# Performance work log

Hardware: AMD Instinct MI355X
Metric: run time of the kernel (lower is better)

Reference implementation:

```python
import jax, jax.numpy as jnp
import numpy as np
from jax import lax

NUM_HEADS = 4
SIDE = 5  # side_dwconv


def setup_inputs() -> dict:
    key = jax.random.key(0)
    ks = jax.random.split(key, 7)
    B, C, H, W = 2, 128, 56, 56
    return {
        "x": jax.random.normal(ks[0], (B, C, H, W), dtype=jnp.float32),
        "qkv_w": jax.random.normal(ks[1], (3 * C, C), dtype=jnp.float32) * 0.02,
        "qkv_b": jax.random.normal(ks[2], (3 * C,), dtype=jnp.float32) * 0.02,
        "lepe_w": jax.random.normal(ks[3], (C, 1, SIDE, SIDE), dtype=jnp.float32) * 0.02,
        "lepe_b": jax.random.normal(ks[4], (C,), dtype=jnp.float32) * 0.02,
        "proj_w": jax.random.normal(ks[5], (C, C), dtype=jnp.float32) * 0.02,
        "proj_b": jax.random.normal(ks[6], (C,), dtype=jnp.float32) * 0.02,
    }


def reference(x, qkv_w, qkv_b, lepe_w, lepe_b, proj_w, proj_b):
    B, C, H, W = x.shape
    nh = NUM_HEADS
    hd = C // nh
    scale = hd ** (-0.5)
    N = H * W

    # 1x1 conv qkv == channel matmul
    qkv = jnp.einsum('oc,bchw->bohw', qkv_w, x) + qkv_b[None, :, None, None]
    q, k, v = jnp.split(qkv, 3, axis=1)  # each [B, C, H, W]

    qr = q.reshape(B, nh, hd, N)
    kr = k.reshape(B, nh, hd, N)
    vr = v.reshape(B, nh, hd, N)

    # attn = q^T k over head_dim -> [B, nh, N, N]
    attn = jnp.einsum('bhdn,bhdm->bhnm', qr, kr) * scale
    attn = jax.nn.softmax(attn, axis=-1)

    # out = attn @ v^T, then permute back to [B, C, H, W]
    out = jnp.einsum('bhnm,bhdm->bhdn', attn, vr).reshape(B, C, H, W)

    # depthwise LePE conv on v, fused with residual add
    pad = SIDE // 2
    lepe = lax.conv_general_dilated(
        v, lepe_w, window_strides=(1, 1), padding=[(pad, pad), (pad, pad)],
        dimension_numbers=('NCHW', 'OIHW', 'NCHW'), feature_group_count=C,
    ) + lepe_b[None, :, None, None]
    out = out + lepe

    # 1x1 conv proj
    out = jnp.einsum('oc,bchw->bohw', proj_w, out) + proj_b[None, :, None, None]
    return out
```

## Files before the change

### kernel.cpp

```cpp
#include <hip/hip_runtime.h>

typedef __bf16 bf16x8 __attribute__((ext_vector_type(8)));
typedef __bf16 bf16x4 __attribute__((ext_vector_type(4)));
typedef float  f32x4  __attribute__((ext_vector_type(4)));

#define NPIX  3136
#define WIMG  56
#define CCH   128
#define NH    4
#define HD    32
#define NSPLIT 8
#define QSCALE 0.2550565470841439f

#if __has_builtin(__builtin_amdgcn_exp2f)
#define FEXP2(x) __builtin_amdgcn_exp2f(x)
#else
#define FEXP2(x) __expf((x) * 0.6931471805599453f)
#endif


__device__ __forceinline__ int perm_inv(int k) {
    return (((k >> 5) & 1) * 2 + ((k >> 2) & 1)) * 16 + (((k >> 3) & 3) * 4) + (k & 3);
}

__global__ __launch_bounds__(256) void k_qkv(
    const float* __restrict__ x, const float* __restrict__ qkv_w,
    const float* __restrict__ qkv_b,
    __bf16* __restrict__ qT, __bf16* __restrict__ kT,
    __bf16* __restrict__ vT, __bf16* __restrict__ vP)
{
    __shared__ __bf16 xl[64][136];
    const int tid = threadIdx.x;
    const int w = tid >> 6, lane = tid & 63;
    const int col = lane & 15, g = lane >> 4;
    const int px0 = blockIdx.x * 64;
    const int slab = blockIdx.y;
    const int b = blockIdx.z;
    const int obase = slab * 128 + w * 32;

    {
        const int px = tid & 63, cq = tid >> 6;
        const float* xp = x + (size_t)b * CCH * NPIX + px0 + px;
        #pragma unroll
        for (int i = 0; i < 8; ++i) {
            const int c0 = cq * 4 + i * 16;
            const float v0 = xp[(size_t)(c0 + 0) * NPIX];
            const float v1 = xp[(size_t)(c0 + 1) * NPIX];
            const float v2 = xp[(size_t)(c0 + 2) * NPIX];
            const float v3 = xp[(size_t)(c0 + 3) * NPIX];
            bf16x4 bv = {(__bf16)v0, (__bf16)v1, (__bf16)v2, (__bf16)v3};
            *(bf16x4*)&xl[px][c0] = bv;
        }
    }
    __syncthreads();

    f32x4 acc[2][4];
    #pragma unroll
    for (int ot = 0; ot < 2; ++ot)
        #pragma unroll
        for (int a = 0; a < 4; ++a) acc[ot][a] = (f32x4){0.f, 0.f, 0.f, 0.f};

    #pragma unroll
    for (int ks = 0; ks < 4; ++ks) {
        const int c0 = ks * 32 + g * 8;
        #pragma unroll
        for (int ot = 0; ot < 2; ++ot) {
            const float* wrow = qkv_w + (size_t)(obase + ot * 16 + col) * CCH + c0;
            const float4 wA = *(const float4*)(wrow);
            const float4 wB = *(const float4*)(wrow + 4);
            bf16x8 af = {(__bf16)wA.x, (__bf16)wA.y, (__bf16)wA.z, (__bf16)wA.w,
                         (__bf16)wB.x, (__bf16)wB.y, (__bf16)wB.z, (__bf16)wB.w};
            #pragma unroll
            for (int a = 0; a < 4; ++a) {
                const bf16x8 bf_ = *(const bf16x8*)&xl[16 * a + col][c0];
                acc[ot][a] = __builtin_amdgcn_mfma_f32_16x16x32_bf16(af, bf_, acc[ot][a], 0, 0, 0);
            }
        }
    }

    #pragma unroll
    for (int ot = 0; ot < 2; ++ot) {
        const int orow = obase + ot * 16 + g * 4;
        const f32x4 bias4 = *(const f32x4*)(qkv_b + orow);
        if (slab == 0) {
            const int o = orow, h = o >> 5, d0 = o & 31;
            __bf16* dst = qT + ((size_t)(b * NH + h) * NPIX) * HD + d0;
            #pragma unroll
            for (int a = 0; a < 4; ++a) {
                const int px = px0 + 16 * a + col;
                bf16x4 v;
                #pragma unroll
                for (int r = 0; r < 4; ++r) v[r] = (__bf16)((acc[ot][a][r] + bias4[r]) * QSCALE);
                *(bf16x4*)(dst + (size_t)px * HD) = v;
            }
        } else if (slab == 1) {
            const int o = orow - 128, h = o >> 5, d0 = o & 31;
            __bf16* dst = kT + ((size_t)(b * NH + h) * NPIX) * HD + d0;
            #pragma unroll
            for (int a = 0; a < 4; ++a) {
                const int s = perm_inv(16 * a + col);
                bf16x4 v;
                #pragma unroll
                for (int r = 0; r < 4; ++r) v[r] = (__bf16)(acc[ot][a][r] + bias4[r]);
                *(bf16x4*)(dst + (size_t)(px0 + s) * HD) = v;
            }
        } else {
            const int c = orow - 256;
            #pragma unroll
            for (int a = 0; a < 4; ++a) {
                const int px = px0 + 16 * a + col;
                const int s = perm_inv(16 * a + col);
                bf16x4 v;
                #pragma unroll
                for (int r = 0; r < 4; ++r) v[r] = (__bf16)(acc[ot][a][r] + bias4[r]);
                *(bf16x4*)(vT + ((size_t)(b * NPIX + px)) * CCH + c) = v;
                #pragma unroll
                for (int r = 0; r < 4; ++r)
                    vP[((size_t)(b * CCH + c + r)) * NPIX + px0 + s] = v[r];
            }
        }
    }
}

__global__ __launch_bounds__(256) void k_attn(
    const __bf16* __restrict__ qT, const __bf16* __restrict__ kT,
    const __bf16* __restrict__ vP,
    __bf16* __restrict__ pO, float* __restrict__ pl)
{
    const int tid = threadIdx.x;
    const int w = tid >> 6, lane = tid & 63;
    const int col = lane & 15, g = lane >> 4;
    const int qt = blockIdx.x;
    const int bh = blockIdx.y;
    const int sp = blockIdx.z * 4 + w;
    const int b = bh >> 2, h = bh & 3;
    const int qbase = qt * 64;
    const size_t headoff = (size_t)bh * NPIX * HD;
    const int c0h = h * HD;

    const __bf16* qbp = qT + headoff + (size_t)(qbase + col) * HD + g * 8;
    const bf16x8 aq0 = *(const bf16x8*)(qbp);
    const bf16x8 aq1 = *(const bf16x8*)(qbp + 16 * HD);
    const bf16x8 aq2 = *(const bf16x8*)(qbp + 32 * HD);
    const bf16x8 aq3 = *(const bf16x8*)(qbp + 48 * HD);

    const __bf16 one = (__bf16)1.0f;
    const bf16x8 ones = {one, one, one, one, one, one, one, one};

    f32x4 O00 = {0,0,0,0}, O01 = {0,0,0,0}, O10 = {0,0,0,0}, O11 = {0,0,0,0};
    f32x4 O20 = {0,0,0,0}, O21 = {0,0,0,0}, O30 = {0,0,0,0}, O31 = {0,0,0,0};
    f32x4 La0 = {0,0,0,0}, La1 = {0,0,0,0}, La2 = {0,0,0,0}, La3 = {0,0,0,0};

    const __bf16* kTh   = kT + headoff;
    const __bf16* vrow0 = vP + (size_t)(b * CCH + c0h + col)      * NPIX;
    const __bf16* vrow1 = vP + (size_t)(b * CCH + c0h + 16 + col) * NPIX;

    const int cs = (49 * sp) >> 3, ce = (49 * (sp + 1)) >> 3;

#define LOADK4(K0R, K1R, K2R, K3R, CHUNK) do { const int _k0 = (CHUNK) * 64;           \
        K0R = *(const bf16x8*)(kTh + (size_t)(_k0      + col) * HD + g * 8);           \
        K1R = *(const bf16x8*)(kTh + (size_t)(_k0 + 16 + col) * HD + g * 8);           \
        K2R = *(const bf16x8*)(kTh + (size_t)(_k0 + 32 + col) * HD + g * 8);           \
        K3R = *(const bf16x8*)(kTh + (size_t)(_k0 + 48 + col) * HD + g * 8); } while (0)

#define SQH(AQ, O0R, O1R, LAR)  do {                                                   \
        f32x4 s0 = __builtin_amdgcn_mfma_f32_16x16x32_bf16(ck0, AQ, zz, 0, 0, 0);      \
        f32x4 s1 = __builtin_amdgcn_mfma_f32_16x16x32_bf16(ck1, AQ, zz, 0, 0, 0);      \
        f32x4 s2 = __builtin_amdgcn_mfma_f32_16x16x32_bf16(ck2, AQ, zz, 0, 0, 0);      \
        f32x4 s3 = __builtin_amdgcn_mfma_f32_16x16x32_bf16(ck3, AQ, zz, 0, 0, 0);      \
        bf16x8 P0 = {(__bf16)FEXP2(s0[0]), (__bf16)FEXP2(s0[1]),                       \
                     (__bf16)FEXP2(s0[2]), (__bf16)FEXP2(s0[3]),                       \
                     (__bf16)FEXP2(s1[0]), (__bf16)FEXP2(s1[1]),                       \
                     (__bf16)FEXP2(s1[2]), (__bf16)FEXP2(s1[3])};                      \
        bf16x8 P1 = {(__bf16)FEXP2(s2[0]), (__bf16)FEXP2(s2[1]),                       \
                     (__bf16)FEXP2(s2[2]), (__bf16)FEXP2(s2[3]),                       \
                     (__bf16)FEXP2(s3[0]), (__bf16)FEXP2(s3[1]),                       \
                     (__bf16)FEXP2(s3[2]), (__bf16)FEXP2(s3[3])};                      \
        O0R = __builtin_amdgcn_mfma_f32_16x16x32_bf16(vv00, P0, O0R, 0, 0, 0);         \
        O0R = __builtin_amdgcn_mfma_f32_16x16x32_bf16(vv01, P1, O0R, 0, 0, 0);         \
        O1R = __builtin_amdgcn_mfma_f32_16x16x32_bf16(vv10, P0, O1R, 0, 0, 0);         \
        O1R = __builtin_amdgcn_mfma_f32_16x16x32_bf16(vv11, P1, O1R, 0, 0, 0);         \
        LAR = __builtin_amdgcn_mfma_f32_16x16x32_bf16(ones, P0, LAR, 0, 0, 0);         \
        LAR = __builtin_amdgcn_mfma_f32_16x16x32_bf16(ones, P1, LAR, 0, 0, 0);         \
    } while (0)

#define CHUNK_STEP(K0R, K1R, K2R, K3R, CHUNK) do {                                     \
        const int _kv0 = (CHUNK) * 64;                                                 \
        const bf16x8 vv00 = *(const bf16x8*)(vrow0 + _kv0      + g * 8);               \
        const bf16x8 vv01 = *(const bf16x8*)(vrow0 + _kv0 + 32 + g * 8);               \
        const bf16x8 vv10 = *(const bf16x8*)(vrow1 + _kv0      + g * 8);               \
        const bf16x8 vv11 = *(const bf16x8*)(vrow1 + _kv0 + 32 + g * 8);               \
        const bf16x8 ck0 = K0R, ck1 = K1R, ck2 = K2R, ck3 = K3R;                       \
        const f32x4 zz = {0.f, 0.f, 0.f, 0.f};                                         \
        SQH(aq0, O00, O01, La0);                                                       \
        SQH(aq1, O10, O11, La1);                                                       \
        SQH(aq2, O20, O21, La2);                                                       \
        SQH(aq3, O30, O31, La3);                                                       \
    } while (0)

    bf16x8 ka0, ka1, ka2, ka3, kb0, kb1, kb2, kb3;
    LOADK4(ka0, ka1, ka2, ka3, cs);
    int cc = cs;
    while (cc + 2 <= ce) {
        LOADK4(kb0, kb1, kb2, kb3, cc + 1);
        CHUNK_STEP(ka0, ka1, ka2, ka3, cc);
        LOADK4(ka0, ka1, ka2, ka3, (cc + 2 < ce) ? cc + 2 : cs);
        CHUNK_STEP(kb0, kb1, kb2, kb3, cc + 1);
        cc += 2;
    }
    if (cc < ce) CHUNK_STEP(ka0, ka1, ka2, ka3, cc);
#undef LOADK4
#undef SQH
#undef CHUNK_STEP

    const int t = bh * 49 + qt;
    __bf16* po = pO + ((size_t)t * NSPLIT + sp) * 64 * 32;
    float* plp = pl + ((size_t)t * NSPLIT + sp) * 64;
#define STQH(QH, O0R, O1R, LAR) do {                                                   \
        bf16x4 v0 = {(__bf16)O0R[0], (__bf16)O0R[1], (__bf16)O0R[2], (__bf16)O0R[3]};  \
        bf16x4 v1 = {(__bf16)O1R[0], (__bf16)O1R[1], (__bf16)O1R[2], (__bf16)O1R[3]};  \
        *(bf16x4*)(po + ((QH) * 16 + col) * 32      + g * 4) = v0;                     \
        *(bf16x4*)(po + ((QH) * 16 + col) * 32 + 16 + g * 4) = v1;                     \
        if (g == 0) plp[(QH) * 16 + col] = LAR[0];                                     \
    } while (0)
    STQH(0, O00, O01, La0);
    STQH(1, O10, O11, La1);
    STQH(2, O20, O21, La2);
    STQH(3, O30, O31, La3);
#undef STQH
}

__global__ __launch_bounds__(256) void k_reduce(
    const __bf16* __restrict__ pO, const float* __restrict__ pl,
    const __bf16* __restrict__ vT,
    const float* __restrict__ lepe_w, const float* __restrict__ lepe_b,
    __bf16* __restrict__ attnT)
{
    __shared__ float wl[32][25];
    __shared__ float bl[32];
    const int tid = threadIdx.x;
    const int qt = blockIdx.x, bh = blockIdx.y;
    const int b = bh >> 2, h = bh & 3;
    const int c0h = h * HD;

    for (int i = tid; i < 800; i += 256) ((float*)wl)[i] = lepe_w[c0h * 25 + i];
    if (tid < 32) bl[tid] = lepe_b[c0h + tid];
    __syncthreads();

    const int q  = tid >> 2;
    const int dg = (tid & 3) * 8;
    const size_t t = (size_t)bh * 49 + qt;

    float lt = 0.f;
    float o[8] = {0.f, 0.f, 0.f, 0.f, 0.f, 0.f, 0.f, 0.f};
    #pragma unroll
    for (int s = 0; s < NSPLIT; ++s) {
        lt += pl[(t * NSPLIT + s) * 64 + q];
        const bf16x8 pv = *(const bf16x8*)(pO + ((t * NSPLIT + s) * 64 + q) * 32 + dg);
        #pragma unroll
        for (int i = 0; i < 8; ++i) o[i] += (float)pv[i];
    }
    const float linv = 1.0f / lt;
    #pragma unroll
    for (int i = 0; i < 8; ++i) o[i] = o[i] * linv + bl[dg + i];

    const int px = qt * 64 + q;
    const int py = px / WIMG, pxx = px % WIMG;
    const __bf16* vtb = vT + ((size_t)b * NPIX) * CCH + c0h + dg;
    #pragma unroll
    for (int dy = 0; dy < 5; ++dy) {
        const int yy = py + dy - 2;
        if (yy < 0 || yy >= WIMG) continue;
        #pragma unroll
        for (int dx = 0; dx < 5; ++dx) {
            const int xx = pxx + dx - 2;
            if (xx < 0 || xx >= WIMG) continue;
            const bf16x8 vv = *(const bf16x8*)(vtb + (size_t)(yy * WIMG + xx) * CCH);
            const int tap = dy * 5 + dx;
            #pragma unroll
            for (int i = 0; i < 8; ++i) o[i] += (float)vv[i] * wl[dg + i][tap];
        }
    }
    bf16x8 ov = {(__bf16)o[0], (__bf16)o[1], (__bf16)o[2], (__bf16)o[3],
                 (__bf16)o[4], (__bf16)o[5], (__bf16)o[6], (__bf16)o[7]};
    *(bf16x8*)(attnT + ((size_t)(b * NPIX + px)) * CCH + c0h + dg) = ov;
}

__global__ __launch_bounds__(256) void k_proj(
    const __bf16* __restrict__ attnT, const float* __restrict__ proj_w,
    const float* __restrict__ proj_b, float* __restrict__ out)
{
    const int tid = threadIdx.x;
    const int w = tid >> 6, lane = tid & 63;
    const int col = lane & 15, g = lane >> 4;
    const int px0 = blockIdx.x * 32 + (w >> 1) * 16;
    const int obase = blockIdx.y * 32 + (w & 1) * 16;
    const int b = blockIdx.z;

    const float* wrow = proj_w + (size_t)(obase + col) * CCH;
    const __bf16* abase = attnT + (size_t)(b * NPIX + px0) * CCH;

    f32x4 acc = {0.f, 0.f, 0.f, 0.f};
    #pragma unroll
    for (int ks = 0; ks < 4; ++ks) {
        const int c0 = ks * 32 + g * 8;
        const float4 wA = *(const float4*)(wrow + c0);
        const float4 wB = *(const float4*)(wrow + c0 + 4);
        bf16x8 af = {(__bf16)wA.x, (__bf16)wA.y, (__bf16)wA.z, (__bf16)wA.w,
                     (__bf16)wB.x, (__bf16)wB.y, (__bf16)wB.z, (__bf16)wB.w};
        const bf16x8 bf_ = *(const bf16x8*)(abase + (size_t)col * CCH + c0);
        acc = __builtin_amdgcn_mfma_f32_16x16x32_bf16(af, bf_, acc, 0, 0, 0);
    }

    const f32x4 pb = *(const f32x4*)(proj_b + obase + g * 4);
    #pragma unroll
    for (int r = 0; r < 4; ++r)
        out[(size_t)(b * CCH + obase + g * 4 + r) * NPIX + px0 + col] = acc[r] + pb[r];
}

extern "C" void kernel_launch(void* const* d_in, const int* in_sizes, int n_in,
                              void* d_out, int out_size, void* d_ws, size_t ws_size,
                              hipStream_t stream)
{
    const float* x      = (const float*)d_in[0];
    const float* qkv_w  = (const float*)d_in[1];
    const float* qkv_b  = (const float*)d_in[2];
    const float* lepe_w = (const float*)d_in[3];
    const float* lepe_b = (const float*)d_in[4];
    const float* proj_w = (const float*)d_in[5];
    const float* proj_b = (const float*)d_in[6];
    float* out = (float*)d_out;

    char* p = (char*)d_ws;
    __bf16* qT    = (__bf16*)p;  p += (size_t)2 * NH * NPIX * HD * 2;
    __bf16* kT    = (__bf16*)p;  p += (size_t)2 * NH * NPIX * HD * 2;
    __bf16* vT    = (__bf16*)p;  p += (size_t)2 * NPIX * CCH * 2;
    __bf16* vP    = (__bf16*)p;  p += (size_t)2 * CCH * NPIX * 2;
    __bf16* attnT = (__bf16*)p;  p += (size_t)2 * NPIX * CCH * 2;
    __bf16* pO    = (__bf16*)p;  p += (size_t)392 * NSPLIT * 64 * 32 * 2;
    float*  pl    = (float*)p;

    k_qkv   <<<dim3(49, 3, 2), dim3(256), 0, stream>>>(x, qkv_w, qkv_b, qT, kT, vT, vP);
    k_attn  <<<dim3(49, 8, 2), dim3(256), 0, stream>>>(qT, kT, vP, pO, pl);
    k_reduce<<<dim3(49, 8),    dim3(256), 0, stream>>>(pO, pl, vT, lepe_w, lepe_b, attnT);
    k_proj  <<<dim3(98, 4, 2), dim3(256), 0, stream>>>(attnT, proj_w, proj_b, out);
}
```

Baseline: 123.2 us.

## Share K/V chunks across four query tiles via double-buffered LDS in attention

After: 122.0 us. About the same (-1.0%).

```diff
diff --git a/kernel.cpp b/kernel.cpp
--- a/kernel.cpp
+++ b/kernel.cpp
@@ -127,14 +127,18 @@
     const __bf16* __restrict__ vP,
     __bf16* __restrict__ pO, float* __restrict__ pl)
 {
+    __shared__ __bf16 Kl[2][64][32];
+    __shared__ __bf16 Vl[2][32][72];
+
     const int tid = threadIdx.x;
     const int w = tid >> 6, lane = tid & 63;
     const int col = lane & 15, g = lane >> 4;
-    const int qt = blockIdx.x;
-    const int bh = blockIdx.y;
-    const int sp = blockIdx.z * 4 + w;
+    const int qt = blockIdx.x * 4 + w;
+    const bool valid = qt < 49;
+    const int qtc = valid ? qt : 48;
+    const int bh = blockIdx.y, sp = blockIdx.z;
     const int b = bh >> 2, h = bh & 3;
-    const int qbase = qt * 64;
+    const int qbase = qtc * 64;
     const size_t headoff = (size_t)bh * NPIX * HD;
     const int c0h = h * HD;
 
@@ -151,17 +155,18 @@
     f32x4 O20 = {0,0,0,0}, O21 = {0,0,0,0}, O30 = {0,0,0,0}, O31 = {0,0,0,0};
     f32x4 La0 = {0,0,0,0}, La1 = {0,0,0,0}, La2 = {0,0,0,0}, La3 = {0,0,0,0};
 
-    const __bf16* kTh   = kT + headoff;
-    const __bf16* vrow0 = vP + (size_t)(b * CCH + c0h + col)      * NPIX;
-    const __bf16* vrow1 = vP + (size_t)(b * CCH + c0h + 16 + col) * NPIX;
+    const __bf16* kTh = kT + headoff;
+    const int vr = tid >> 3;
+    const int vo = (tid & 7) * 8;
+    const __bf16* vsrc = vP + (size_t)(b * CCH + c0h + vr) * NPIX + vo;
 
     const int cs = (49 * sp) >> 3, ce = (49 * (sp + 1)) >> 3;
 
-#define LOADK4(K0R, K1R, K2R, K3R, CHUNK) do { const int _k0 = (CHUNK) * 64;           \
-        K0R = *(const bf16x8*)(kTh + (size_t)(_k0      + col) * HD + g * 8);           \
-        K1R = *(const bf16x8*)(kTh + (size_t)(_k0 + 16 + col) * HD + g * 8);           \
-        K2R = *(const bf16x8*)(kTh + (size_t)(_k0 + 32 + col) * HD + g * 8);           \
-        K3R = *(const bf16x8*)(kTh + (size_t)(_k0 + 48 + col) * HD + g * 8); } while (0)
+#define STAGE(BUF, CHUNK) do { const int _k0 = (CHUNK) * 64;                           \
+        *(bf16x8*)(&Kl[BUF][0][0] + tid * 8) =                                         \
+            *(const bf16x8*)(kTh + (size_t)_k0 * HD + tid * 8);                        \
+        *(bf16x8*)(&Vl[BUF][vr][vo]) = *(const bf16x8*)(vsrc + _k0);                   \
+    } while (0)
 
 #define SQH(AQ, O0R, O1R, LAR)  do {                                                   \
         f32x4 s0 = __builtin_amdgcn_mfma_f32_16x16x32_bf16(ck0, AQ, zz, 0, 0, 0);      \
@@ -184,13 +189,17 @@
         LAR = __builtin_amdgcn_mfma_f32_16x16x32_bf16(ones, P1, LAR, 0, 0, 0);         \
     } while (0)
 
-#define CHUNK_STEP(K0R, K1R, K2R, K3R, CHUNK) do {                                     \
-        const int _kv0 = (CHUNK) * 64;                                                 \
-        const bf16x8 vv00 = *(const bf16x8*)(vrow0 + _kv0      + g * 8);               \
-        const bf16x8 vv01 = *(const bf16x8*)(vrow0 + _kv0 + 32 + g * 8);               \
-        const bf16x8 vv10 = *(const bf16x8*)(vrow1 + _kv0      + g * 8);               \
-        const bf16x8 vv11 = *(const bf16x8*)(vrow1 + _kv0 + 32 + g * 8);               \
-        const bf16x8 ck0 = K0R, ck1 = K1R, ck2 = K2R, ck3 = K3R;                       \
+#define COMPUTE(CUR) do {                                                              \
+        const __bf16* Kb = &Kl[CUR][0][0];                                             \
+        const __bf16* Vb = &Vl[CUR][0][0];                                             \
+        const bf16x8 ck0 = *(const bf16x8*)(Kb + (      col) * 32 + g * 8);            \
+        const bf16x8 ck1 = *(const bf16x8*)(Kb + (16 + col) * 32 + g * 8);             \
+        const bf16x8 ck2 = *(const bf16x8*)(Kb + (32 + col) * 32 + g * 8);             \
+        const bf16x8 ck3 = *(const bf16x8*)(Kb + (48 + col) * 32 + g * 8);             \
+        const bf16x8 vv00 = *(const bf16x8*)(Vb + (      col) * 72      + g * 8);      \
+        const bf16x8 vv01 = *(const bf16x8*)(Vb + (      col) * 72 + 32 + g * 8);      \
+        const bf16x8 vv10 = *(const bf16x8*)(Vb + (16 + col) * 72      + g * 8);       \
+        const bf16x8 vv11 = *(const bf16x8*)(Vb + (16 + col) * 72 + 32 + g * 8);       \
         const f32x4 zz = {0.f, 0.f, 0.f, 0.f};                                         \
         SQH(aq0, O00, O01, La0);                                                       \
         SQH(aq1, O10, O11, La1);                                                       \
@@ -198,21 +207,19 @@
         SQH(aq3, O30, O31, La3);                                                       \
     } while (0)
 
-    bf16x8 ka0, ka1, ka2, ka3, kb0, kb1, kb2, kb3;
-    LOADK4(ka0, ka1, ka2, ka3, cs);
-    int cc = cs;
-    while (cc + 2 <= ce) {
-        LOADK4(kb0, kb1, kb2, kb3, cc + 1);
-        CHUNK_STEP(ka0, ka1, ka2, ka3, cc);
-        LOADK4(ka0, ka1, ka2, ka3, (cc + 2 < ce) ? cc + 2 : cs);
-        CHUNK_STEP(kb0, kb1, kb2, kb3, cc + 1);
-        cc += 2;
-    }
-    if (cc < ce) CHUNK_STEP(ka0, ka1, ka2, ka3, cc);
-#undef LOADK4
+    STAGE(0, cs);
+    __syncthreads();
+    for (int cc = cs; cc < ce; ++cc) {
+        const int cur = (cc - cs) & 1;
+        if (cc + 1 < ce) STAGE(cur ^ 1, cc + 1);
+        COMPUTE(cur);
+        __syncthreads();
+    }
+#undef STAGE
 #undef SQH
-#undef CHUNK_STEP
-
+#undef COMPUTE
+
+    if (!valid) return;
     const int t = bh * 49 + qt;
     __bf16* po = pO + ((size_t)t * NSPLIT + sp) * 64 * 32;
     float* plp = pl + ((size_t)t * NSPLIT + sp) * 64;
@@ -341,7 +348,7 @@
     float*  pl    = (float*)p;
 
     k_qkv   <<<dim3(49, 3, 2), dim3(256), 0, stream>>>(x, qkv_w, qkv_b, qT, kT, vT, vP);
-    k_attn  <<<dim3(49, 8, 2), dim3(256), 0, stream>>>(qT, kT, vP, pO, pl);
+    k_attn  <<<dim3(13, 8, 8), dim3(256), 0, stream>>>(qT, kT, vP, pO, pl);
     k_reduce<<<dim3(49, 8),    dim3(256), 0, stream>>>(pO, pl, vT, lepe_w, lepe_b, attnT);
     k_proj  <<<dim3(98, 4, 2), dim3(256), 0, stream>>>(attnT, proj_w, proj_b, out);
 }
```
